# Kernel optimization log

Measured on AMD Instinct MI355X. Metric: run time of the kernel, lower is better.

## Reference

```python
import jax, jax.numpy as jnp
import numpy as np
from jax import lax

B = 256          # batch
E = 512          # encoder_dim
P = 512          # prefix_size = latent_dim
D = 768          # gpt_embedding_size (dim_embedding)
H = 8            # num_heads (hard-coded in TransformerMapper)
DH = D // H
CL = 40          # clip_length (time_length)
PL = 40          # prefix_length
L = 8            # num_layers
MH = int(D * 2.0)  # mlp hidden, mlp_ratio=2.0
EPS = 1e-5


def setup_inputs() -> dict:
    key = jax.random.key(0)
    ks = jax.random.split(key, 20)
    s = 0.02
    inp = {
        "latent": jax.random.normal(ks[0], (B, E), jnp.float32),
        # model.linear: encoder_dim -> prefix_size
        "lin_w": jax.random.normal(ks[1], (E, P), jnp.float32) * s,
        "lin_b": jnp.zeros((P,), jnp.float32),
        # TransformerMapper.linear: dim_clip -> clip_length * dim_embedding
        "map_w": jax.random.normal(ks[2], (P, CL * D), jnp.float32) * s,
        "map_b": jnp.zeros((CL * D,), jnp.float32),
        "prefix_const": jax.random.normal(ks[3], (PL, D), jnp.float32),
        # per-layer params, stacked along leading layer dim L
        "ln1_s": jnp.ones((L, D), jnp.float32),
        "ln1_b": jnp.zeros((L, D), jnp.float32),
        "wq": jax.random.normal(ks[4], (L, D, D), jnp.float32) * s,
        "wkv": jax.random.normal(ks[5], (L, D, 2 * D), jnp.float32) * s,
        "wo": jax.random.normal(ks[6], (L, D, D), jnp.float32) * s,
        "bo": jnp.zeros((L, D), jnp.float32),
        "ln2_s": jnp.ones((L, D), jnp.float32),
        "ln2_b": jnp.zeros((L, D), jnp.float32),
        "w1": jax.random.normal(ks[7], (L, D, MH), jnp.float32) * s,
        "b1": jnp.zeros((L, MH), jnp.float32),
        "w2": jax.random.normal(ks[8], (L, MH, D), jnp.float32) * s,
        "b2": jnp.zeros((L, D), jnp.float32),
    }
    return inp


def _layernorm(x, scale, bias):
    m = jnp.mean(x, axis=-1, keepdims=True)
    v = jnp.mean(jnp.square(x - m), axis=-1, keepdims=True)
    return (x - m) * lax.rsqrt(v + EPS) * scale + bias


def _transformer(x, layer_params):
    scale = DH ** (-0.5)

    def layer(x, p):
        (l1s, l1b, wq, wkv, wo, bo, l2s, l2b, w1, b1, w2, b2) = p
        b, n, c = x.shape
        h = _layernorm(x, l1s, l1b)
        q = (h @ wq).reshape(b, n, H, DH)
        kv = (h @ wkv).reshape(b, n, 2, H, DH)
        k, v = kv[:, :, 0], kv[:, :, 1]
        att = jnp.einsum('bnhd,bmhd->bnmh', q, k) * scale
        att = jax.nn.softmax(att, axis=2)  # softmax over keys (dim m)
        o = jnp.einsum('bnmh,bmhd->bnhd', att, v).reshape(b, n, c)
        x = x + o @ wo + bo
        h2 = _layernorm(x, l2s, l2b)
        x = x + jax.nn.relu(h2 @ w1 + b1) @ w2 + b2
        return x, None

    x, _ = lax.scan(layer, x, layer_params)
    return x


def reference(latent, lin_w, lin_b, map_w, map_b, prefix_const,
              ln1_s, ln1_b, wq, wkv, wo, bo, ln2_s, ln2_b, w1, b1, w2, b2):
    # CldTextDecoder.forward core math (up to prefix_embed)
    lat = latent @ lin_w + lin_b                      # [B, P]
    x = (lat @ map_w + map_b).reshape(B, CL, D)       # TransformerMapper.linear
    pre = jnp.broadcast_to(prefix_const[None], (B, PL, D))
    seq = jnp.concatenate([x, pre], axis=1)           # [B, CL+PL, D]
    layer_params = (ln1_s, ln1_b, wq, wkv, wo, bo, ln2_s, ln2_b, w1, b1, w2, b2)
    out = _transformer(seq, layer_params)[:, CL:]     # [B, PL, D]
    return out
```

## Files before the change

kernel.cpp:

```cpp
#include <hip/hip_runtime.h>
#include <hip/hip_bf16.h>
#include <stdint.h>

typedef __bf16 bf16;
typedef unsigned int uint;
typedef __attribute__((ext_vector_type(8))) __bf16 bf16x8;
typedef __attribute__((ext_vector_type(4))) float floatx4;

#define DEV static __device__ __forceinline__

typedef const __attribute__((address_space(1))) void* gptr_t;
typedef __attribute__((address_space(3))) void* lptr_t;

DEV void gload16(const void* g, void* l) {
  __builtin_amdgcn_global_load_lds((gptr_t)g, (lptr_t)l, 16, 0, 0);
}

DEV uint f2b2(float x, float y) {
  union { bf16 h[2]; uint u; } pk;
  pk.h[0] = (bf16)x; pk.h[1] = (bf16)y;
  return pk.u;
}

#define EP_STORE_BF16 0
#define EP_STORE_F32  1
#define EP_ACCUM_F32  2
#define EP_RELU_BF16  3
#define EP_QKV        4

template<int MODE>
__global__ __launch_bounds__(256, 4)
void gemm_bt(const bf16* __restrict__ A, const bf16* __restrict__ Bt,
             void* __restrict__ Cv, void* __restrict__ Cv2,
             const float* __restrict__ bias, int K, int ldc)
{
  __shared__ bf16 As[128 * 64];
  __shared__ bf16 Bs[128 * 64];
  const int tid  = threadIdx.x;
  const int wave = tid >> 6;
  const int lane = tid & 63;

  int bx = blockIdx.x, by = blockIdx.y;
  const int gx = (int)gridDim.x, gy = (int)gridDim.y;
  if ((gy & 7) == 0) {
    const int flat = by * gx + bx;
    const int xcd  = flat & 7;
    const int s    = flat >> 3;
    const int rows_per = gy >> 3;
    const int m_local  = s / gx;
    bx = s - m_local * gx;
    by = xcd * rows_per + m_local;
  }
  const int m0 = by * 128;
  const int n0 = bx * 128;
  const int wm = (wave >> 1) * 64;
  const int wn = (wave & 1) * 64;

  const int rA = tid >> 3;
  const int lc = (tid & 7) ^ (rA & 7);
  const bf16* Asrc = A  + (size_t)(m0 + rA) * K + lc * 8;
  const bf16* Bsrc = Bt + (size_t)(n0 + rA) * K + lc * 8;
  bf16* Adst = As + tid * 8;
  bf16* Bdst = Bs + tid * 8;

  floatx4 acc[4][4] = {};
  const int quad = lane >> 4;
  const int lrow = lane & 15;
  const int xr   = lrow & 7;

  for (int k0 = 0; k0 < K; k0 += 64) {
#pragma unroll
    for (int j = 0; j < 4; j++) {
      gload16(Asrc + k0 + (size_t)j * 32 * K, Adst + j * 2048);
      gload16(Bsrc + k0 + (size_t)j * 32 * K, Bdst + j * 2048);
    }
    __syncthreads();

#pragma unroll
    for (int ks = 0; ks < 2; ks++) {
      bf16x8 af[4], bfr[4];
#pragma unroll
      for (int i = 0; i < 4; i++)
        af[i] = *(const bf16x8*)(As + (wm + i * 16 + lrow) * 64 + ((ks * 4 + quad) ^ xr) * 8);
#pragma unroll
      for (int j = 0; j < 4; j++)
        bfr[j] = *(const bf16x8*)(Bs + (wn + j * 16 + lrow) * 64 + ((ks * 4 + quad) ^ xr) * 8);
#pragma unroll
      for (int i = 0; i < 4; i++)
#pragma unroll
        for (int j = 0; j < 4; j++)
          acc[i][j] = __builtin_amdgcn_mfma_f32_16x16x32_bf16(af[i], bfr[j], acc[i][j], 0, 0, 0);
    }
    __syncthreads();
  }

#pragma unroll
  for (int i = 0; i < 4; i++) {
    const int gm_base = m0 + wm + i * 16 + quad * 4;
#pragma unroll
    for (int j = 0; j < 4; j++) {
      const int gn = n0 + wn + j * 16 + lrow;
      const float bv = (MODE != EP_QKV && bias) ? bias[gn] : 0.f;
#pragma unroll
      for (int r = 0; r < 4; r++) {
        const int gm = gm_base + r;
        float val = acc[i][j][r] + bv;
        if (MODE == EP_QKV) {
          if (gn < 768) ((bf16*)Cv)[(size_t)gm * 768 + gn] = (bf16)val;
          else          ((bf16*)Cv2)[(size_t)gm * 1536 + (gn - 768)] = (bf16)val;
        } else {
          const size_t idx = (size_t)gm * ldc + gn;
          if (MODE == EP_STORE_BF16)      ((bf16*)Cv)[idx] = (bf16)val;
          else if (MODE == EP_STORE_F32)  ((float*)Cv)[idx] = val;
          else if (MODE == EP_ACCUM_F32)  ((float*)Cv)[idx] += val;
          else { val = val > 0.f ? val : 0.f; ((bf16*)Cv)[idx] = (bf16)val; }
        }
      }
    }
  }
}

__global__ __launch_bounds__(256)
void transpose_cast(const float* __restrict__ in, bf16* __restrict__ out,
                    int K, int N, int n_off)
{
  __shared__ float t[64][65];
  const int n0 = blockIdx.x * 64, k0 = blockIdx.y * 64;
  const int c  = threadIdx.x & 63;
  const int r4 = threadIdx.x >> 6;
#pragma unroll
  for (int p = 0; p < 16; p++) {
    const int r = p * 4 + r4;
    t[r][c] = in[(size_t)(k0 + r) * N + n_off + n0 + c];
  }
  __syncthreads();
#pragma unroll
  for (int p = 0; p < 16; p++) {
    const int r = p * 4 + r4;
    out[(size_t)(n0 + r) * K + k0 + c] = (bf16)t[c][r];
  }
}

__global__ __launch_bounds__(256)
void ln_kernel(const float* __restrict__ x, const float* __restrict__ sc,
               const float* __restrict__ bi, bf16* __restrict__ h)
{
  const int wave = threadIdx.x >> 6, lane = threadIdx.x & 63;
  const size_t row = (size_t)blockIdx.x * 4 + wave;
  const float* xr = x + row * 768;
  float4 v[3];
  float sum = 0.f;
#pragma unroll
  for (int i = 0; i < 3; i++) {
    v[i] = *(const float4*)(xr + i * 256 + lane * 4);
    sum += v[i].x + v[i].y + v[i].z + v[i].w;
  }
#pragma unroll
  for (int off = 32; off > 0; off >>= 1) sum += __shfl_xor(sum, off, 64);
  const float mean = sum * (1.f / 768.f);
  float sq = 0.f;
#pragma unroll
  for (int i = 0; i < 3; i++) {
    const float a = v[i].x - mean, b = v[i].y - mean;
    const float c = v[i].z - mean, d = v[i].w - mean;
    sq += a * a + b * b + c * c + d * d;
  }
#pragma unroll
  for (int off = 32; off > 0; off >>= 1) sq += __shfl_xor(sq, off, 64);
  const float inv = rsqrtf(sq * (1.f / 768.f) + 1e-5f);
  bf16* hr = h + row * 768;
#pragma unroll
  for (int i = 0; i < 3; i++) {
    const int p = i * 256 + lane * 4;
    const float4 s4 = *(const float4*)(sc + p);
    const float4 b4 = *(const float4*)(bi + p);
    union { bf16 b[4]; uint2 u; } pk;
    pk.b[0] = (bf16)((v[i].x - mean) * inv * s4.x + b4.x);
    pk.b[1] = (bf16)((v[i].y - mean) * inv * s4.y + b4.y);
    pk.b[2] = (bf16)((v[i].z - mean) * inv * s4.z + b4.z);
    pk.b[3] = (bf16)((v[i].w - mean) * inv * s4.w + b4.w);
    *(uint2*)(hr + p) = pk.u;
  }
}

__global__ __launch_bounds__(256, 2)
void attn_kernel(const bf16* __restrict__ q, const bf16* __restrict__ kv,
                 bf16* __restrict__ o)
{
  __shared__ __align__(16) char smem[76032];
  bf16*  Qls = (bf16*)smem;
  bf16*  Kls = (bf16*)(smem + 15360);
  bf16*  Vt  = (bf16*)(smem + 30720);
  float* S   = (float*)(smem + 49152);
  bf16*  P   = Qls;

  const int tid = threadIdx.x;
  const int wave = tid >> 6, lane = tid & 63;
  const int quad = lane >> 4, lrow = lane & 15;
  const int b = blockIdx.x >> 3, hh = blockIdx.x & 7;
  const bf16* qbp = q  + (size_t)b * 80 * 768  + hh * 96;
  const bf16* kbp = kv + (size_t)b * 80 * 1536 + hh * 96;
  const bf16* vbp = kbp + 768;
  bf16* obp = o + (size_t)b * 80 * 768 + hh * 96;

  for (int i = tid; i < 3840; i += 256) {
    const int n = i / 48, dp = i - n * 48;
    ((uint*)Qls)[i] = *(const uint*)(qbp + (size_t)n * 768  + dp * 2);
    ((uint*)Kls)[i] = *(const uint*)(kbp + (size_t)n * 1536 + dp * 2);
    union { uint u; bf16 h[2]; } v;
    v.u = *(const uint*)(vbp + (size_t)n * 1536 + dp * 2);
    Vt[(2 * dp)     * 96 + n] = v.h[0];
    Vt[(2 * dp + 1) * 96 + n] = v.h[1];
  }
  for (int i = tid; i < 768; i += 256) {
    const int n = i >> 3, kp = i & 7;
    ((uint*)Vt)[n * 48 + 40 + kp] = 0u;
  }
  __syncthreads();

  const float scale = 0.1020620726159658f;
  for (int t = wave; t < 25; t += 4) {
    const int mi = t / 5, ni = t - (t / 5) * 5;
    floatx4 acc = {};
#pragma unroll
    for (int ks = 0; ks < 3; ks++) {
      const bf16x8 a  = *(const bf16x8*)(Qls + (mi * 16 + lrow) * 96 + ks * 32 + quad * 8);
      const bf16x8 bb = *(const bf16x8*)(Kls + (ni * 16 + lrow) * 96 + ks * 32 + quad * 8);
      acc = __builtin_amdgcn_mfma_f32_16x16x32_bf16(a, bb, acc, 0, 0, 0);
    }
#pragma unroll
    for (int r = 0; r < 4; r++)
      S[(mi * 16 + quad * 4 + r) * 84 + ni * 16 + lrow] = acc[r] * scale;
  }
  __syncthreads();

  if (tid < 80) {
    float* sr = S + tid * 84;
    float mx = -1e30f;
    for (int m = 0; m < 80; m++) mx = fmaxf(mx, sr[m]);
    float sm = 0.f;
    for (int m = 0; m < 80; m++) { const float e = __expf(sr[m] - mx); sr[m] = e; sm += e; }
    const float inv = 1.f / sm;
    uint* pr = (uint*)(P + tid * 96);
    for (int m = 0; m < 40; m++) pr[m] = f2b2(sr[2 * m] * inv, sr[2 * m + 1] * inv);
    for (int m = 40; m < 48; m++) pr[m] = 0u;
  }
  __syncthreads();

  for (int t = wave; t < 30; t += 4) {
    const int mi = t / 6, ni = t - (t / 6) * 6;
    floatx4 acc = {};
#pragma unroll
    for (int ks = 0; ks < 3; ks++) {
      const bf16x8 a  = *(const bf16x8*)(P  + (mi * 16 + lrow) * 96 + ks * 32 + quad * 8);
      const bf16x8 bb = *(const bf16x8*)(Vt + (ni * 16 + lrow) * 96 + ks * 32 + quad * 8);
      acc = __builtin_amdgcn_mfma_f32_16x16x32_bf16(a, bb, acc, 0, 0, 0);
    }
#pragma unroll
    for (int r = 0; r < 4; r++)
      obp[(size_t)(mi * 16 + quad * 4 + r) * 768 + ni * 16 + lrow] = (bf16)acc[r];
  }
}

__global__ __launch_bounds__(256)
void cast_f2b(const float* __restrict__ in, bf16* __restrict__ out, int n4)
{
  const int i = blockIdx.x * 256 + threadIdx.x;
  if (i >= n4) return;
  const float4 v = *(const float4*)(in + (size_t)i * 4);
  union { bf16 b[4]; uint2 u; } pk;
  pk.b[0] = (bf16)v.x; pk.b[1] = (bf16)v.y; pk.b[2] = (bf16)v.z; pk.b[3] = (bf16)v.w;
  *(uint2*)(out + (size_t)i * 4) = pk.u;
}

__global__ __launch_bounds__(256)
void prefix_fill(const float* __restrict__ pre, float* __restrict__ x)
{
  const size_t i = (size_t)blockIdx.x * 256 + threadIdx.x;
  const size_t b = i / 7680, r = i - b * 7680;
  *(float4*)(x + b * 61440 + 30720 + r * 4) = *(const float4*)(pre + r * 4);
}

__global__ __launch_bounds__(256)
void copy_out(const float* __restrict__ x, float* __restrict__ out)
{
  const size_t i = (size_t)blockIdx.x * 256 + threadIdx.x;
  const size_t b = i / 7680, r = i - b * 7680;
  *(float4*)(out + b * 30720 + r * 4) = *(const float4*)(x + b * 61440 + 30720 + r * 4);
}

extern "C" void kernel_launch(void* const* d_in, const int* in_sizes, int n_in,
                              void* d_out, int out_size, void* d_ws, size_t ws_size,
                              hipStream_t stream)
{
  (void)in_sizes; (void)n_in; (void)out_size;
  const float* latent = (const float*)d_in[0];
  const float* lin_w  = (const float*)d_in[1];
  const float* lin_b  = (const float*)d_in[2];
  const float* map_w  = (const float*)d_in[3];
  const float* map_b  = (const float*)d_in[4];
  const float* prefix = (const float*)d_in[5];
  const float* ln1_s  = (const float*)d_in[6];
  const float* ln1_b  = (const float*)d_in[7];
  const float* wq     = (const float*)d_in[8];
  const float* wkv    = (const float*)d_in[9];
  const float* wo     = (const float*)d_in[10];
  const float* bo     = (const float*)d_in[11];
  const float* ln2_s  = (const float*)d_in[12];
  const float* ln2_b  = (const float*)d_in[13];
  const float* w1     = (const float*)d_in[14];
  const float* b1     = (const float*)d_in[15];
  const float* w2     = (const float*)d_in[16];
  const float* b2     = (const float*)d_in[17];
  float* out = (float*)d_out;

  int nchunk; bool wt_all;
  if      (ws_size >= 234000000ull) { nchunk = 1; wt_all = true;  }
  else if (ws_size >= 168000000ull) { nchunk = 1; wt_all = false; }
  else if (ws_size >= 121000000ull) { nchunk = 2; wt_all = false; }
  else if (ws_size >=  97000000ull) { nchunk = 4; wt_all = false; }
  else                              { nchunk = 8; wt_all = false; }
  const int Rc = 20480 / nchunk;
  const int Bc = 256 / nchunk;
  const int npiece = (nchunk <= 2) ? 1 : (nchunk == 4 ? 2 : 4);
  const int pieceN = 30720 / npiece;

  char* wsp = (char*)d_ws;
  auto alloc = [&](size_t bytes) -> char* {
    char* p = wsp; wsp += (bytes + 255) & ~(size_t)255; return p;
  };
  float* xw    = (float*)alloc(62914560ull);
  char*  region = alloc((size_t)4608 * Rc);
  char*  wT     = alloc(wt_all ? 75497472ull : 9437184ull);

  bf16* mapT = (bf16*)region;
  char* tail = region + (size_t)pieceN * 512 * 2;
  bf16* latv = (bf16*)tail;
  bf16* latb = (bf16*)(tail + 262144);
  bf16* linT = (bf16*)(tail + 524288);
  bf16* hbuf = (bf16*)region;
  bf16* kvb  = (bf16*)(region + (size_t)Rc * 1536);
  bf16* qb   = (bf16*)d_out;

  const dim3 blk(256);

  cast_f2b<<<128, blk, 0, stream>>>(latent, latv, 32768);
  transpose_cast<<<dim3(8, 8), blk, 0, stream>>>(lin_w, linT, 512, 512, 0);
  gemm_bt<EP_STORE_BF16><<<dim3(4, 2), blk, 0, stream>>>(latv, linT, latb, nullptr, lin_b, 512, 512);
  for (int p = 0; p < npiece; p++) {
    transpose_cast<<<dim3(pieceN / 64, 8), blk, 0, stream>>>(map_w, mapT, 512, 30720, p * pieceN);
    gemm_bt<EP_STORE_F32><<<dim3(pieceN / 128, 2), blk, 0, stream>>>(
        latb, mapT, xw + p * pieceN, nullptr, map_b + p * pieceN, 512, 61440);
  }
  prefix_fill<<<7680, blk, 0, stream>>>(prefix, xw);

  if (wt_all) {
    for (int l = 0; l < 8; l++) {
      char* wl = wT + (size_t)l * 9437184;
      transpose_cast<<<dim3(12, 12), blk, 0, stream>>>(wq + (size_t)l * 589824,  (bf16*)wl,             768, 768, 0);
      transpose_cast<<<dim3(24, 12), blk, 0, stream>>>(wkv + (size_t)l * 1179648,(bf16*)(wl + 1179648), 768, 1536, 0);
      transpose_cast<<<dim3(12, 12), blk, 0, stream>>>(wo + (size_t)l * 589824,  (bf16*)(wl + 3538944), 768, 768, 0);
      transpose_cast<<<dim3(24, 12), blk, 0, stream>>>(w1 + (size_t)l * 1179648, (bf16*)(wl + 4718592), 768, 1536, 0);
      transpose_cast<<<dim3(12, 24), blk, 0, stream>>>(w2 + (size_t)l * 1179648, (bf16*)(wl + 7077888), 1536, 768, 0);
    }
  }

  for (int l = 0; l < 8; l++) {
    char* wl = wT + (wt_all ? (size_t)l * 9437184 : 0);
    bf16* wqT  = (bf16*)wl;
    bf16* woT  = (bf16*)(wl + 3538944);
    bf16* w1T  = (bf16*)(wl + 4718592);
    bf16* w2T  = (bf16*)(wl + 7077888);
    if (!wt_all) {
      transpose_cast<<<dim3(12, 12), blk, 0, stream>>>(wq + (size_t)l * 589824,  wqT,  768, 768, 0);
      transpose_cast<<<dim3(24, 12), blk, 0, stream>>>(wkv + (size_t)l * 1179648,(bf16*)(wl + 1179648), 768, 1536, 0);
      transpose_cast<<<dim3(12, 12), blk, 0, stream>>>(wo + (size_t)l * 589824,  woT,  768, 768, 0);
      transpose_cast<<<dim3(24, 12), blk, 0, stream>>>(w1 + (size_t)l * 1179648, w1T,  768, 1536, 0);
      transpose_cast<<<dim3(12, 24), blk, 0, stream>>>(w2 + (size_t)l * 1179648, w2T,  1536, 768, 0);
    }
    for (int c = 0; c < nchunk; c++) {
      float* xc = xw + (size_t)c * Rc * 768;
      ln_kernel<<<Rc / 4, blk, 0, stream>>>(xc, ln1_s + l * 768, ln1_b + l * 768, hbuf);
      gemm_bt<EP_QKV><<<dim3(18, Rc / 128), blk, 0, stream>>>(
          hbuf, wqT, qb, kvb, nullptr, 768, 0);
      attn_kernel<<<Bc * 8, blk, 0, stream>>>(qb, kvb, qb);
      gemm_bt<EP_ACCUM_F32><<<dim3(6, Rc / 128), blk, 0, stream>>>(
          qb, woT, xc, nullptr, bo + l * 768, 768, 768);
      ln_kernel<<<Rc / 4, blk, 0, stream>>>(xc, ln2_s + l * 768, ln2_b + l * 768, hbuf);
      gemm_bt<EP_RELU_BF16><<<dim3(12, Rc / 128), blk, 0, stream>>>(
          hbuf, w1T, kvb, nullptr, b1 + l * 1536, 768, 1536);
      gemm_bt<EP_ACCUM_F32><<<dim3(6, Rc / 128), blk, 0, stream>>>(
          kvb, w2T, xc, nullptr, b2 + l * 768, 1536, 768);
    }
  }
  copy_out<<<7680, blk, 0, stream>>>(xw, out);
}
```

Before: 3.079 ms.

## Add 256x256-tile 8-wave GEMM with phased LDS pipeline for transformer layers

Adds a new GEMM kernel using 256x256 output tiles, 512 threads, double-buffered LDS loaded via direct global-to-LDS loads, and a four-phase interleave of LDS reads, prefetches and MFMA blocks with priority hints. It also remaps block indices so row groups stay on the same XCD. All four per-layer GEMMs (QKV, out-proj, MLP up, MLP down) switch to it, aiming for more data reuse per tile and better overlap of loads with compute. The larger tiles mean fewer blocks (e.g. 3 column tiles for the N=768 GEMMs), which risks underfilling the GPU when the chunk size Rc is small, and 128 KB of LDS per block limits occupancy.

```diff
diff --git a/kernel.cpp b/kernel.cpp
--- a/kernel.cpp
+++ b/kernel.cpp
@@ -96,6 +96,154 @@
 
 #pragma unroll
   for (int i = 0; i < 4; i++) {
+    const int gm_base = m0 + wm + i * 16 + quad * 4;
+#pragma unroll
+    for (int j = 0; j < 4; j++) {
+      const int gn = n0 + wn + j * 16 + lrow;
+      const float bv = (MODE != EP_QKV && bias) ? bias[gn] : 0.f;
+#pragma unroll
+      for (int r = 0; r < 4; r++) {
+        const int gm = gm_base + r;
+        float val = acc[i][j][r] + bv;
+        if (MODE == EP_QKV) {
+          if (gn < 768) ((bf16*)Cv)[(size_t)gm * 768 + gn] = (bf16)val;
+          else          ((bf16*)Cv2)[(size_t)gm * 1536 + (gn - 768)] = (bf16)val;
+        } else {
+          const size_t idx = (size_t)gm * ldc + gn;
+          if (MODE == EP_STORE_BF16)      ((bf16*)Cv)[idx] = (bf16)val;
+          else if (MODE == EP_STORE_F32)  ((float*)Cv)[idx] = val;
+          else if (MODE == EP_ACCUM_F32)  ((float*)Cv)[idx] += val;
+          else { val = val > 0.f ? val : 0.f; ((bf16*)Cv)[idx] = (bf16)val; }
+        }
+      }
+    }
+  }
+}
+
+#define SBAR()  __builtin_amdgcn_s_barrier()
+#define LGKM0() asm volatile("s_waitcnt lgkmcnt(0)" ::: "memory")
+
+#define PH_MFMA(AF, BF, MO)                                                    \
+  _Pragma("unroll")                                                            \
+  for (int m = 0; m < 4; m++) {                                                \
+    _Pragma("unroll")                                                          \
+    for (int n = 0; n < 4; n++)                                                \
+      acc[MO + m][n] =                                                         \
+        __builtin_amdgcn_mfma_f32_16x16x32_bf16(AF[m], BF[n], acc[MO + m][n],  \
+                                                0, 0, 0);                      \
+  }
+
+template<int MODE>
+__global__ __launch_bounds__(512, 2)
+void gemm256(const bf16* __restrict__ A, const bf16* __restrict__ Bt,
+             void* __restrict__ Cv, void* __restrict__ Cv2,
+             const float* __restrict__ bias, int K, int ldc)
+{
+  __shared__ __align__(16) bf16 sm[2][32768];
+
+  const int tid  = threadIdx.x;
+  const int wave = tid >> 6;
+  const int lane = tid & 63;
+  const int quad = lane >> 4;
+  const int lrow = lane & 15;
+  const int xr   = lrow & 7;
+  const int wm   = (wave >> 2) * 128;
+  const int wn   = (wave & 3) * 64;
+
+  int bx = blockIdx.x, by = blockIdx.y;
+  const int gx = (int)gridDim.x, gy = (int)gridDim.y;
+  if ((gy & 7) == 0) {
+    const int flat = by * gx + bx;
+    const int xcd  = flat & 7;
+    const int s    = flat >> 3;
+    const int rows_per = gy >> 3;
+    const int m_local  = s / gx;
+    bx = s - m_local * gx;
+    by = xcd * rows_per + m_local;
+  }
+  const int m0 = by * 256;
+  const int n0 = bx * 256;
+
+  const int rA = tid >> 3;
+  const int lc = (tid & 7) ^ (rA & 7);
+  const bf16* Ag = A  + (size_t)(m0 + rA) * K + lc * 8;
+  const bf16* Bg = Bt + (size_t)(n0 + rA) * K + lc * 8;
+  const int NT = K >> 6;
+
+  auto stA = [&](int buf, int t) {
+    const bf16* s = Ag + t * 64;
+    bf16* d = &sm[buf][tid * 8];
+    gload16(s,                   d);
+    gload16(s + (size_t)64  * K, d + 4096);
+    gload16(s + (size_t)128 * K, d + 8192);
+    gload16(s + (size_t)192 * K, d + 12288);
+  };
+  auto stB = [&](int buf, int t, int h) {
+    const bf16* s = Bg + t * 64 + (size_t)(h * 128) * K;
+    bf16* d = &sm[buf][16384 + h * 8192 + tid * 8];
+    gload16(s,                  d);
+    gload16(s + (size_t)64 * K, d + 4096);
+  };
+
+  floatx4 acc[8][4] = {};
+  const int c0 = ((0 + quad) ^ xr) * 8;
+  const int c1 = ((4 + quad) ^ xr) * 8;
+  const int ar = (wm + lrow) * 64;
+  const int br = (wn + lrow) * 64;
+
+  stA(0, 0); stB(0, 0, 0); stB(0, 0, 1); stA(1, 1);
+  asm volatile("s_waitcnt vmcnt(4)" ::: "memory");
+  SBAR();
+
+  for (int t = 0; t < NT; ++t) {
+    const int cur = t & 1, nxt = cur ^ 1;
+    const bf16* sa = sm[cur];
+    const bf16* sb = sm[cur] + 16384;
+    bf16x8 b0[4], b1[4], aA[4], aB[4], aC[4], aD[4];
+
+#pragma unroll
+    for (int n = 0; n < 4; n++) b0[n] = *(const bf16x8*)(sb + br + n * 1024 + c0);
+#pragma unroll
+    for (int m = 0; m < 4; m++) aA[m] = *(const bf16x8*)(sa + ar + m * 1024 + c0);
+#pragma unroll
+    for (int m = 0; m < 4; m++) aB[m] = *(const bf16x8*)(sa + ar + m * 1024 + c1);
+    if (t + 1 < NT) stB(nxt, t + 1, 0);
+    SBAR(); LGKM0();
+    __builtin_amdgcn_s_setprio(1);
+    PH_MFMA(aA, b0, 0)
+    __builtin_amdgcn_s_setprio(0);
+    SBAR();
+
+#pragma unroll
+    for (int m = 0; m < 4; m++) aC[m] = *(const bf16x8*)(sa + ar + 4096 + m * 1024 + c0);
+#pragma unroll
+    for (int m = 0; m < 4; m++) aD[m] = *(const bf16x8*)(sa + ar + 4096 + m * 1024 + c1);
+    if (t + 1 < NT) stB(nxt, t + 1, 1);
+    SBAR(); LGKM0();
+    __builtin_amdgcn_s_setprio(1);
+    PH_MFMA(aC, b0, 4)
+    __builtin_amdgcn_s_setprio(0);
+    SBAR();
+
+#pragma unroll
+    for (int n = 0; n < 4; n++) b1[n] = *(const bf16x8*)(sb + br + n * 1024 + c1);
+    if (t + 2 < NT) stA(cur, t + 2);
+    SBAR(); LGKM0();
+    __builtin_amdgcn_s_setprio(1);
+    PH_MFMA(aB, b1, 0)
+    __builtin_amdgcn_s_setprio(0);
+    SBAR();
+
+    __builtin_amdgcn_s_setprio(1);
+    PH_MFMA(aD, b1, 4)
+    __builtin_amdgcn_s_setprio(0);
+    if (t + 2 < NT) { asm volatile("s_waitcnt vmcnt(4)" ::: "memory"); }
+    else            { asm volatile("s_waitcnt vmcnt(0)" ::: "memory"); }
+    SBAR();
+  }
+
+#pragma unroll
+  for (int i = 0; i < 8; i++) {
     const int gm_base = m0 + wm + i * 16 + quad * 4;
 #pragma unroll
     for (int j = 0; j < 4; j++) {
@@ -343,6 +491,7 @@
   bf16* qb   = (bf16*)d_out;
 
   const dim3 blk(256);
+  const dim3 blk5(512);
 
   cast_f2b<<<128, blk, 0, stream>>>(latent, latv, 32768);
   transpose_cast<<<dim3(8, 8), blk, 0, stream>>>(lin_w, linT, 512, 512, 0);
@@ -381,15 +530,15 @@
     for (int c = 0; c < nchunk; c++) {
       float* xc = xw + (size_t)c * Rc * 768;
       ln_kernel<<<Rc / 4, blk, 0, stream>>>(xc, ln1_s + l * 768, ln1_b + l * 768, hbuf);
-      gemm_bt<EP_QKV><<<dim3(18, Rc / 128), blk, 0, stream>>>(
+      gemm256<EP_QKV><<<dim3(9, Rc / 256), blk5, 0, stream>>>(
           hbuf, wqT, qb, kvb, nullptr, 768, 0);
       attn_kernel<<<Bc * 8, blk, 0, stream>>>(qb, kvb, qb);
-      gemm_bt<EP_ACCUM_F32><<<dim3(6, Rc / 128), blk, 0, stream>>>(
+      gemm256<EP_ACCUM_F32><<<dim3(3, Rc / 256), blk5, 0, stream>>>(
           qb, woT, xc, nullptr, bo + l * 768, 768, 768);
       ln_kernel<<<Rc / 4, blk, 0, stream>>>(xc, ln2_s + l * 768, ln2_b + l * 768, hbuf);
-      gemm_bt<EP_RELU_BF16><<<dim3(12, Rc / 128), blk, 0, stream>>>(
+      gemm256<EP_RELU_BF16><<<dim3(6, Rc / 256), blk5, 0, stream>>>(
           hbuf, w1T, kvb, nullptr, b1 + l * 1536, 768, 1536);
-      gemm_bt<EP_ACCUM_F32><<<dim3(6, Rc / 128), blk, 0, stream>>>(
+      gemm256<EP_ACCUM_F32><<<dim3(3, Rc / 256), blk5, 0, stream>>>(
           kvb, w2T, xc, nullptr, b2 + l * 768, 1536, 768);
     }
   }
```

After: 3.338 ms. 8.4% more time.
